# Optimization experiments

Measured on AMD Instinct MI355X. Metric: run time of the kernel, lower is better.

The kernel has to match this reference:

```python
import jax, jax.numpy as jnp
import numpy as np
from jax import lax

EPS = 1e-5
F_IN, F_OUT, R = 128, 256, 16
B, H, W = 16, 128, 128


def _conv(x, w, stride):
    # x: [B,C,H,W], w: [O,I,kh,kw]; ME convs keep coordinates -> SAME padding
    return lax.conv_general_dilated(x, w, (stride, stride), 'SAME',
                                    dimension_numbers=('NCHW', 'OIHW', 'NCHW'))


def _bn(x, g, b, m, v):
    scale = g * lax.rsqrt(v + EPS)
    return x * scale[None, :, None, None] + (b - m * scale)[None, :, None, None]


def setup_inputs() -> dict:
    key = jax.random.key(0)
    ks = jax.random.split(key, 12)
    d = {}
    d['x'] = jax.random.normal(ks[0], (B, F_IN, H, W), jnp.float32)
    # BatchNorm params (eval mode running stats)
    d['bn1_g'] = jax.random.uniform(ks[1], (F_IN,), jnp.float32, 0.5, 1.5)
    d['bn1_b'] = jax.random.normal(ks[2], (F_IN,), jnp.float32) * 0.1
    d['bn1_m'] = jax.random.normal(ks[3], (F_IN,), jnp.float32) * 0.1
    d['bn1_v'] = jax.random.uniform(ks[4], (F_IN,), jnp.float32, 0.5, 1.5)
    d['bn2_g'] = jax.random.uniform(ks[5], (F_OUT,), jnp.float32, 0.5, 1.5)
    d['bn2_b'] = jax.random.normal(ks[6], (F_OUT,), jnp.float32) * 0.1
    d['bn2_m'] = jax.random.normal(ks[7], (F_OUT,), jnp.float32) * 0.1
    d['bn2_v'] = jax.random.uniform(ks[8], (F_OUT,), jnp.float32, 0.5, 1.5)
    # Conv weights (no bias, ME default)
    d['w_conv1'] = jax.random.normal(ks[9], (F_OUT, F_IN, 3, 3), jnp.float32) * (1.0 / np.sqrt(9 * F_IN))
    d['w_conv2'] = jax.random.normal(ks[10], (F_OUT, F_OUT, 3, 3), jnp.float32) * (1.0 / np.sqrt(9 * F_OUT))
    d['w_res'] = jax.random.normal(ks[11], (F_OUT, F_IN, 1, 1), jnp.float32) * (1.0 / np.sqrt(F_IN))
    # SE block linears
    k12, k13, k14, k15 = jax.random.split(jax.random.fold_in(key, 1), 4)
    d['se_w1'] = jax.random.normal(k12, (F_OUT // R, F_OUT), jnp.float32) * (1.0 / np.sqrt(F_OUT))
    d['se_b1'] = jax.random.normal(k13, (F_OUT // R,), jnp.float32) * 0.01
    d['se_w2'] = jax.random.normal(k14, (F_OUT, F_OUT // R), jnp.float32) * (1.0 / np.sqrt(F_OUT // R))
    d['se_b2'] = jax.random.normal(k15, (F_OUT,), jnp.float32) * 0.01
    return d


def reference(x, bn1_g, bn1_b, bn1_m, bn1_v, bn2_g, bn2_b, bn2_m, bn2_v,
              w_conv1, w_conv2, w_res, se_w1, se_b1, se_w2, se_b2):
    # shared BN+ReLU prefix (self.first_batch / self.first_relu reused)
    pre = jax.nn.relu(_bn(x, bn1_g, bn1_b, bn1_m, bn1_v))
    # residual branch: 1x1 stride-2 conv (f_out > f_in)
    residual = _conv(pre, w_res, 2)
    # main branch
    h = _conv(pre, w_conv1, 2)                          # [B,F_OUT,H/2,W/2]
    h = jax.nn.relu(_bn(h, bn2_g, bn2_b, bn2_m, bn2_v))
    h = _conv(h, w_conv2, 1)
    # SE attention: global avg pool -> FC -> ReLU -> FC -> sigmoid -> scale
    s = jnp.mean(h, axis=(2, 3))                        # [B,F_OUT]
    a = jax.nn.sigmoid(jax.nn.relu(s @ se_w1.T + se_b1) @ se_w2.T + se_b2)
    h = h * a[:, :, None, None]
    return h + residual
```

## Files before the change

### kernel.cpp

```cpp
#include <hip/hip_runtime.h>

typedef unsigned short u16;
typedef __attribute__((ext_vector_type(8))) unsigned short u16x8;
typedef __attribute__((ext_vector_type(8))) __bf16 bf16x8;
typedef __attribute__((ext_vector_type(4))) float f32x4;

__device__ __forceinline__ float bf2f(u16 u) {
    return __uint_as_float(((unsigned)u) << 16);
}
__device__ __forceinline__ u16 f2bf(float f) {
    unsigned u = __float_as_uint(f);
    return (u16)((u + 0x7FFFu + ((u >> 16) & 1u)) >> 16);
}

__global__ void setup_kernel(const float* __restrict__ w1, const float* __restrict__ w2,
                             const float* __restrict__ wr,
                             const float* __restrict__ g2, const float* __restrict__ b2,
                             const float* __restrict__ m2, const float* __restrict__ v2,
                             u16* __restrict__ w1t, u16* __restrict__ w2t,
                             u16* __restrict__ wrt, float* __restrict__ bias2f,
                             u16* __restrict__ pre, u16* __restrict__ h1) {
    int b = blockIdx.x;
    if (b < 3585) {
        int i = b * 256 + threadIdx.x;
        if (i < 294912) {
            int ci = i & 127; int t = i >> 7; int o = t & 255; int tap = t >> 8;
            int dy = tap / 3, dx = tap - dy * 3;
            float sc = g2[o] * rsqrtf(v2[o] + 1e-5f);
            w1t[i] = f2bf(w1[((o * 128 + ci) * 3 + dy) * 3 + dx] * sc);
        } else if (i < 294912 + 589824) {
            int j = i - 294912;
            int ci = j & 255; int t = j >> 8; int o = t & 255; int tap = t >> 8;
            int dy = tap / 3, dx = tap - dy * 3;
            w2t[j] = f2bf(w2[((o * 256 + ci) * 3 + dy) * 3 + dx]);
        } else if (i < 294912 + 589824 + 32768) {
            int j = i - (294912 + 589824);
            int ci = j & 127; int o = j >> 7;
            wrt[j] = f2bf(wr[o * 128 + ci]);
        } else {
            int o = i - (294912 + 589824 + 32768);
            if (o < 256) {
                float sc = g2[o] * rsqrtf(v2[o] + 1e-5f);
                bias2f[o] = b2[o] - m2[o] * sc;
            }
        }
    } else if (b < 3585 + 2056) {
        int i = (b - 3585) * 256 + threadIdx.x;
        if (i < 16 * 129 * 128) {
            int c = i & 127; int t = i >> 7; int n = t / 129; int xx = t - n * 129;
            pre[((n * 129 + 128) * 129 + xx) * 128 + c] = 0;
        } else {
            int j = i - 16 * 129 * 128;
            int c = j & 127; int t = j >> 7; int n = t >> 7; int y = t & 127;
            pre[((n * 129 + y) * 129 + 128) * 128 + c] = 0;
        }
    } else {
        int i = (b - (3585 + 2056)) * 256 + threadIdx.x;
        int c = i & 255;
        int t = i >> 8;
        int n = t / 260;
        int cl = t - n * 260;
        int y, x;
        if (cl < 66)       { y = 0;  x = cl; }
        else if (cl < 132) { y = 65; x = cl - 66; }
        else if (cl < 196) { x = 0;  y = cl - 131; }
        else               { x = 65; y = cl - 195; }
        h1[((n * 66 + y) * 66 + x) * 256 + c] = 0;
    }
}

__global__ void pre_kernel(const float* __restrict__ x, const float* __restrict__ g,
                           const float* __restrict__ b, const float* __restrict__ m,
                           const float* __restrict__ v, u16* __restrict__ pre) {
    __shared__ u16 tile[128 * 136];
    int n = blockIdx.x >> 7, y = blockIdx.x & 127;
    int tid = threadIdx.x;
    int c = tid >> 1, xh = (tid & 1) << 6;
    float sc = g[c] * rsqrtf(v[c] + 1e-5f);
    float bi = b[c] - m[c] * sc;
    const float4* src = (const float4*)(x + (((n * 128 + c) * 128 + y) << 7) + xh);
#pragma unroll
    for (int j = 0; j < 16; ++j) {
        float4 val = src[j];
        int xb = xh + j * 4;
        tile[(xb + 0) * 136 + c] = f2bf(fmaxf(val.x * sc + bi, 0.f));
        tile[(xb + 1) * 136 + c] = f2bf(fmaxf(val.y * sc + bi, 0.f));
        tile[(xb + 2) * 136 + c] = f2bf(fmaxf(val.z * sc + bi, 0.f));
        tile[(xb + 3) * 136 + c] = f2bf(fmaxf(val.w * sc + bi, 0.f));
    }
    __syncthreads();
    int c0 = (tid & 15) << 3;
#pragma unroll
    for (int xi = 0; xi < 8; ++xi) {
        int xx = xi * 16 + (tid >> 4);
        u16x8 val = *(const u16x8*)&tile[xx * 136 + c0];
        *(u16x8*)(pre + ((n * 129 + y) * 129 + xx) * 128 + c0) = val;
    }
}

template <int CIN, int NTAPS, int STRIDE, bool BIASRELU, bool POOL>
__global__ __launch_bounds__(512, 2)
void conv_8ph(const u16* __restrict__ in, const u16* __restrict__ wt,
              const float* __restrict__ bias, u16* __restrict__ out,
              float* __restrict__ pool_out,
              int in_row, int in_img, int out_base, int out_row, int out_img) {
    constexpr int CSTEPS = CIN / 64;
    constexpr int KT = CSTEPS * NTAPS;
    __shared__ __attribute__((aligned(16))) u16 lds[81920];

    const int tid = threadIdx.x;
    const int w = tid >> 6, l = tid & 63;
    const int wm = w >> 2, wn = w & 3;
    const int l15 = l & 15;
    const int bid = ((blockIdx.x & 7) << 5) | (blockIdx.x >> 3);
    const int Mbase = bid << 8;

    const int srow = tid >> 3;
    const int swze = (((tid & 7) ^ (srow & 7)) << 3);
    int pix0 = Mbase + srow;
    int nn0 = pix0 >> 12, p0 = (pix0 >> 6) & 63, q0 = pix0 & 63;
    const int abase0 = nn0 * in_img + (STRIDE * p0) * in_row + (STRIDE * q0) * CIN + swze;
    const int astep = STRIDE * in_row;
    const int bbase0 = srow * CIN + swze;
    const int bstep = 64 * CIN;

    int colw[2];
#pragma unroll
    for (int kk = 0; kk < 2; ++kk)
        colw[kk] = (kk * 32 + (l >> 4) * 8) ^ ((l & 7) << 3);

    f32x4 acc[8][4] = {};
    bf16x8 afr[4][2], bXf[2][2], bYf[2][2];

#define AOFF(ks) (((NTAPS == 9) ? ((((ks) / CSTEPS) / 3) * in_row + (((ks) / CSTEPS) % 3) * CIN) : 0) + ((ks) % CSTEPS) * 64)
#define BOFF(ks) (((ks) / CSTEPS) * 256 * CIN + ((ks) % CSTEPS) * 64)
#define GLDS(gsrc, ldst) __builtin_amdgcn_global_load_lds(                          \
        (__attribute__((address_space(1))) void*)(gsrc),                            \
        (__attribute__((address_space(3))) void*)(ldst), 16, 0, 0)
#define STAGE_A(base, h, ks) {                                                      \
    int _ao = AOFF(ks);                                                             \
    GLDS(in + abase0 + (2 * (h) + 0) * astep + _ao,                                 \
         &lds[(base) + (h) * 8192 + 0 * 4096 + w * 512]);                           \
    GLDS(in + abase0 + (2 * (h) + 1) * astep + _ao,                                 \
         &lds[(base) + (h) * 8192 + 1 * 4096 + w * 512]); }
#define STAGE_B(base, h, ks) {                                                      \
    int _bo = BOFF(ks);                                                             \
    GLDS(wt + bbase0 + (2 * (h) + 0) * bstep + _bo,                                 \
         &lds[(base) + (h) * 8192 + 0 * 4096 + w * 512]);                           \
    GLDS(wt + bbase0 + (2 * (h) + 1) * bstep + _bo,                                 \
         &lds[(base) + (h) * 8192 + 1 * 4096 + w * 512]); }
#define BARRIER() { __builtin_amdgcn_s_barrier(); asm volatile("" ::: "memory"); }
#define LDA(base, MH) {                                                             \
    _Pragma("unroll") for (int fm = 0; fm < 4; ++fm)                                \
    _Pragma("unroll") for (int kk = 0; kk < 2; ++kk)                                \
        afr[fm][kk] = *(const bf16x8*)&lds[(base) + ((MH) * 128 + wm * 64 + fm * 16 + l15) * 64 + colw[kk]]; }
#define LDB(base, NH, dst) {                                                        \
    _Pragma("unroll") for (int gn = 0; gn < 2; ++gn)                                \
    _Pragma("unroll") for (int kk = 0; kk < 2; ++kk)                                \
        dst[gn][kk] = *(const bf16x8*)&lds[(base) + ((NH) * 128 + gn * 64 + wn * 16 + l15) * 64 + colw[kk]]; }
#define MFMA_Q(MH, NH, bset) {                                                      \
    _Pragma("unroll") for (int fm = 0; fm < 4; ++fm)                                \
    _Pragma("unroll") for (int gn = 0; gn < 2; ++gn)                                \
    _Pragma("unroll") for (int kk = 0; kk < 2; ++kk)                                \
        acc[(MH) * 4 + fm][(NH) * 2 + gn] = __builtin_amdgcn_mfma_f32_16x16x32_bf16( \
            afr[fm][kk], bset[gn][kk], acc[(MH) * 4 + fm][(NH) * 2 + gn], 0, 0, 0); }

    STAGE_A(0, 0, 0); STAGE_A(0, 1, 0);
    STAGE_B(49152, 0, 0); STAGE_B(49152, 1, 0);
    STAGE_A(16384, 0, 1); STAGE_A(16384, 1, 1);
    asm volatile("s_waitcnt vmcnt(4)" ::: "memory");
    BARRIER();

    int Ar = 0;
    int As = 32768;
    int Brel = 0;

    LDB(49152, 0, bXf);

#define CBODY(T, B0, B1, STAGEA, VM)                                                \
    {                                                                               \
        const int Br = 49152 + Brel, Bs = 49152 + (Brel ^ 16384);                   \
        LDA(Ar, 0);                                                                 \
        LDB(Br, 1, B1);                                                             \
        STAGE_B(Bs, 0, (T) + 1); STAGE_B(Bs, 1, (T) + 1);                           \
        __builtin_amdgcn_s_setprio(1);                                              \
        MFMA_Q(0, 0, B0);                                                           \
        MFMA_Q(0, 1, B1);                                                           \
        __builtin_amdgcn_s_setprio(0);                                              \
        LDA(Ar, 1);                                                                 \
        if (STAGEA) { STAGE_A(As, 0, (T) + 2); STAGE_A(As, 1, (T) + 2); }           \
        __builtin_amdgcn_s_setprio(1);                                              \
        MFMA_Q(1, 1, B1);                                                           \
        __builtin_amdgcn_s_setprio(0);                                              \
        asm volatile("s_waitcnt vmcnt(" #VM ")" ::: "memory");                      \
        BARRIER();                                                                  \
        LDB(49152 + (Brel ^ 16384), 0, B1);         \
        __builtin_amdgcn_s_setprio(1);                                              \
        MFMA_Q(1, 0, B0);                                   \
        __builtin_amdgcn_s_setprio(0);                                              \
        Ar = (Ar == 32768) ? 0 : Ar + 16384;                                        \
        As = (As == 32768) ? 0 : As + 16384;                                        \
        Brel ^= 16384;                                                              \
    }

#pragma unroll 1
    for (int t = 0; t < KT - 2; t += 2) {
        CBODY(t,     bXf, bYf, true, 4);
        CBODY(t + 1, bYf, bXf, true, 4);
    }

    CBODY(KT - 2, bXf, bYf, false, 0);

    {
        const int Br = 49152 + Brel;
        LDA(Ar, 0);
        LDB(Br, 1, bXf);
        MFMA_Q(0, 0, bYf);
        MFMA_Q(0, 1, bXf);
        LDA(Ar, 1);
        MFMA_Q(1, 1, bXf);
        MFMA_Q(1, 0, bYf);
    }
#undef CBODY
#undef AOFF
#undef BOFF
#undef GLDS
#undef STAGE_A
#undef STAGE_B
#undef LDA
#undef LDB

#pragma unroll
    for (int f = 0; f < 8; ++f) {
        const int prow = (f >> 2) * 128 + wm * 64 + (f & 3) * 16 + ((l >> 4) << 2);
#pragma unroll
        for (int g = 0; g < 4; ++g) {
            const int o = (g >> 1) * 128 + (g & 1) * 64 + wn * 16 + l15;
            float bb = 0.f;
            if (BIASRELU) bb = bias[o];
#pragma unroll
            for (int j = 0; j < 4; ++j) {
                int pix = Mbase + prow + j;
                int nn = pix >> 12, p = (pix >> 6) & 63, q = pix & 63;
                float val = acc[f][g][j] + bb;
                if (BIASRELU) val = fmaxf(val, 0.f);
                out[out_base + nn * out_img + p * out_row + q * 256 + o] = f2bf(val);
            }
        }
    }

    if (POOL) {
        float ps[4];
#pragma unroll
        for (int g = 0; g < 4; ++g) {
            float s = 0.f;
#pragma unroll
            for (int f = 0; f < 8; ++f)
#pragma unroll
                for (int j = 0; j < 4; ++j) s += acc[f][g][j];
            s += __shfl_xor(s, 16);
            s += __shfl_xor(s, 32);
            ps[g] = s;
        }
        asm volatile("s_waitcnt lgkmcnt(0)" ::: "memory");
        BARRIER();
        float* fl = (float*)lds;
        if ((l >> 4) == 0) {
#pragma unroll
            for (int g = 0; g < 4; ++g) {
                int o = (g >> 1) * 128 + (g & 1) * 64 + wn * 16 + l15;
                fl[wm * 256 + o] = ps[g];
            }
        }
        BARRIER();
        if (tid < 256)
            pool_out[bid * 256 + tid] = fl[tid] + fl[256 + tid];
    }
#undef MFMA_Q
#undef BARRIER
}

__global__ void se_kernel(const float* __restrict__ partial,
                          const float* __restrict__ w1, const float* __restrict__ b1,
                          const float* __restrict__ w2, const float* __restrict__ b2,
                          float* __restrict__ a) {
    __shared__ float sm[16 * 256];
    __shared__ float hl[16 * 16];
    int t = threadIdx.x;
    for (int n = 0; n < 16; ++n) {
        float s = 0.f;
#pragma unroll
        for (int k = 0; k < 16; ++k) s += partial[(n * 16 + k) * 256 + t];
        sm[n * 256 + t] = s * (1.0f / 4096.0f);
    }
    __syncthreads();
    {
        int bb = t >> 4, j = t & 15;
        float d = b1[j];
        for (int c = 0; c < 256; ++c) d += sm[bb * 256 + c] * w1[j * 256 + c];
        hl[bb * 16 + j] = fmaxf(d, 0.f);
    }
    __syncthreads();
    {
        int o = t;
        for (int bb = 0; bb < 16; ++bb) {
            float z = b2[o];
            for (int j = 0; j < 16; ++j) z += hl[bb * 16 + j] * w2[o * 16 + j];
            a[bb * 256 + o] = 1.0f / (1.0f + expf(-z));
        }
    }
}

__global__ void finalize_kernel(const u16* __restrict__ h2, const u16* __restrict__ res,
                                const float* __restrict__ a, float* __restrict__ out) {
    __shared__ u16 th[256 * 68];
    __shared__ float al[256];
    int n = blockIdx.x >> 6, p = blockIdx.x & 63;
    int t = threadIdx.x;
    al[t] = a[n * 256 + t];
    __syncthreads();
    int o8 = (t & 31) << 3, qr = t >> 5;
    int pixbase = n * 4096 + p * 64;
#pragma unroll
    for (int qi = 0; qi < 8; ++qi) {
        int q = qi * 8 + qr;
        int gi = (pixbase + q) * 256 + o8;
        u16x8 hv = *(const u16x8*)(h2 + gi);
        u16x8 rv = *(const u16x8*)(res + gi);
#pragma unroll
        for (int k = 0; k < 8; ++k) {
            float vv = bf2f(hv[k]) * al[o8 + k] + bf2f(rv[k]);
            th[(o8 + k) * 68 + q] = f2bf(vv);
        }
    }
    __syncthreads();
    int q4 = (t & 15) << 2, ob = t >> 4;
#pragma unroll
    for (int oi = 0; oi < 16; ++oi) {
        int o = oi * 16 + ob;
        float4 vv;
        vv.x = bf2f(th[o * 68 + q4 + 0]);
        vv.y = bf2f(th[o * 68 + q4 + 1]);
        vv.z = bf2f(th[o * 68 + q4 + 2]);
        vv.w = bf2f(th[o * 68 + q4 + 3]);
        *(float4*)(out + ((n * 256 + o) * 64 + p) * 64 + q4) = vv;
    }
}

static const size_t OFF_PRE  = 0;
static const size_t OFF_H1   = 68161536;
static const size_t OFF_RES  = 103845888;
static const size_t OFF_W1T  = 137400320;
static const size_t OFF_W2T  = 137990144;
static const size_t OFF_WRT  = 139169792;
static const size_t OFF_B2F  = 139235328;
static const size_t OFF_PART = 139236352;
static const size_t OFF_A    = 139760640;

extern "C" void kernel_launch(void* const* d_in, const int* in_sizes, int n_in,
                              void* d_out, int out_size, void* d_ws, size_t ws_size,
                              hipStream_t stream) {
    (void)in_sizes; (void)n_in; (void)out_size; (void)ws_size;
    const float* x      = (const float*)d_in[0];
    const float* bn1_g  = (const float*)d_in[1];
    const float* bn1_b  = (const float*)d_in[2];
    const float* bn1_m  = (const float*)d_in[3];
    const float* bn1_v  = (const float*)d_in[4];
    const float* bn2_g  = (const float*)d_in[5];
    const float* bn2_b  = (const float*)d_in[6];
    const float* bn2_m  = (const float*)d_in[7];
    const float* bn2_v  = (const float*)d_in[8];
    const float* wc1    = (const float*)d_in[9];
    const float* wc2    = (const float*)d_in[10];
    const float* wres   = (const float*)d_in[11];
    const float* se_w1  = (const float*)d_in[12];
    const float* se_b1  = (const float*)d_in[13];
    const float* se_w2  = (const float*)d_in[14];
    const float* se_b2  = (const float*)d_in[15];

    char* ws = (char*)d_ws;
    u16*   pre    = (u16*)(ws + OFF_PRE);
    u16*   h2     = (u16*)(ws + OFF_PRE);
    u16*   h1     = (u16*)(ws + OFF_H1);
    u16*   res    = (u16*)(ws + OFF_RES);
    u16*   w1t    = (u16*)(ws + OFF_W1T);
    u16*   w2t    = (u16*)(ws + OFF_W2T);
    u16*   wrt    = (u16*)(ws + OFF_WRT);
    float* bias2f = (float*)(ws + OFF_B2F);
    float* part   = (float*)(ws + OFF_PART);
    float* avec   = (float*)(ws + OFF_A);
    float* out    = (float*)d_out;

    setup_kernel<<<9801, 256, 0, stream>>>(wc1, wc2, wres, bn2_g, bn2_b, bn2_m, bn2_v,
                                           w1t, w2t, wrt, bias2f, pre, h1);
    pre_kernel<<<2048, 256, 0, stream>>>(x, bn1_g, bn1_b, bn1_m, bn1_v, pre);

    conv_8ph<128, 9, 2, true, false><<<256, 512, 0, stream>>>(
        pre, w1t, bias2f, h1, nullptr,
        129 * 128, 129 * 129 * 128,
        67 * 256, 66 * 256, 66 * 66 * 256);

    conv_8ph<128, 1, 2, false, false><<<256, 512, 0, stream>>>(
        pre, wrt, nullptr, res, nullptr,
        129 * 128, 129 * 129 * 128,
        0, 64 * 256, 4096 * 256);

    conv_8ph<256, 9, 1, false, true><<<256, 512, 0, stream>>>(
        h1, w2t, nullptr, h2, part,
        66 * 256, 66 * 66 * 256,
        0, 64 * 256, 4096 * 256);

    se_kernel<<<1, 256, 0, stream>>>(part, se_w1, se_b1, se_w2, se_b2, avec);
    finalize_kernel<<<1024, 256, 0, stream>>>(h2, res, avec, out);
}
```

Baseline: 209.3 us.

## Fuse residual conv and SE into finalize, merge pre-BN into setup

Folds the BN1+ReLU pre-pass into the setup kernel as extra blocks. Computes the 1x1 stride-2 residual conv inside the finalize kernel with MFMA, so the separate residual launch and its bf16 round trip through global memory go away. The single-block SE kernel is also replaced by per-block SE recomputation in finalize. h2 moves to its own buffer because pre must stay live until finalize, and every finalize block now redundantly repeats the SE math and reads pre and weights directly from global memory without LDS staging.

```diff
diff --git a/kernel.cpp b/kernel.cpp
--- a/kernel.cpp
+++ b/kernel.cpp
@@ -13,13 +13,17 @@
     return (u16)((u + 0x7FFFu + ((u >> 16) & 1u)) >> 16);
 }
 
-__global__ void setup_kernel(const float* __restrict__ w1, const float* __restrict__ w2,
+__global__ void setup_kernel(const float* __restrict__ x,
+                             const float* __restrict__ g1, const float* __restrict__ b1,
+                             const float* __restrict__ m1, const float* __restrict__ v1,
+                             const float* __restrict__ w1, const float* __restrict__ w2,
                              const float* __restrict__ wr,
                              const float* __restrict__ g2, const float* __restrict__ b2,
                              const float* __restrict__ m2, const float* __restrict__ v2,
                              u16* __restrict__ w1t, u16* __restrict__ w2t,
                              u16* __restrict__ wrt, float* __restrict__ bias2f,
                              u16* __restrict__ pre, u16* __restrict__ h1) {
+    __shared__ u16 tile[128 * 136];
     int b = blockIdx.x;
     if (b < 3585) {
         int i = b * 256 + threadIdx.x;
@@ -54,47 +58,43 @@
             int c = j & 127; int t = j >> 7; int n = t >> 7; int y = t & 127;
             pre[((n * 129 + y) * 129 + 128) * 128 + c] = 0;
         }
-    } else {
+    } else if (b < 3585 + 2056 + 4160) {
         int i = (b - (3585 + 2056)) * 256 + threadIdx.x;
         int c = i & 255;
         int t = i >> 8;
         int n = t / 260;
         int cl = t - n * 260;
-        int y, x;
-        if (cl < 66)       { y = 0;  x = cl; }
-        else if (cl < 132) { y = 65; x = cl - 66; }
-        else if (cl < 196) { x = 0;  y = cl - 131; }
-        else               { x = 65; y = cl - 195; }
-        h1[((n * 66 + y) * 66 + x) * 256 + c] = 0;
-    }
-}
-
-__global__ void pre_kernel(const float* __restrict__ x, const float* __restrict__ g,
-                           const float* __restrict__ b, const float* __restrict__ m,
-                           const float* __restrict__ v, u16* __restrict__ pre) {
-    __shared__ u16 tile[128 * 136];
-    int n = blockIdx.x >> 7, y = blockIdx.x & 127;
-    int tid = threadIdx.x;
-    int c = tid >> 1, xh = (tid & 1) << 6;
-    float sc = g[c] * rsqrtf(v[c] + 1e-5f);
-    float bi = b[c] - m[c] * sc;
-    const float4* src = (const float4*)(x + (((n * 128 + c) * 128 + y) << 7) + xh);
-#pragma unroll
-    for (int j = 0; j < 16; ++j) {
-        float4 val = src[j];
-        int xb = xh + j * 4;
-        tile[(xb + 0) * 136 + c] = f2bf(fmaxf(val.x * sc + bi, 0.f));
-        tile[(xb + 1) * 136 + c] = f2bf(fmaxf(val.y * sc + bi, 0.f));
-        tile[(xb + 2) * 136 + c] = f2bf(fmaxf(val.z * sc + bi, 0.f));
-        tile[(xb + 3) * 136 + c] = f2bf(fmaxf(val.w * sc + bi, 0.f));
-    }
-    __syncthreads();
-    int c0 = (tid & 15) << 3;
-#pragma unroll
-    for (int xi = 0; xi < 8; ++xi) {
-        int xx = xi * 16 + (tid >> 4);
-        u16x8 val = *(const u16x8*)&tile[xx * 136 + c0];
-        *(u16x8*)(pre + ((n * 129 + y) * 129 + xx) * 128 + c0) = val;
+        int y, x2;
+        if (cl < 66)       { y = 0;  x2 = cl; }
+        else if (cl < 132) { y = 65; x2 = cl - 66; }
+        else if (cl < 196) { x2 = 0; y = cl - 131; }
+        else               { x2 = 65; y = cl - 195; }
+        h1[((n * 66 + y) * 66 + x2) * 256 + c] = 0;
+    } else {
+        int pb = b - (3585 + 2056 + 4160);
+        int n = pb >> 7, y = pb & 127;
+        int tid = threadIdx.x;
+        int c = tid >> 1, xh = (tid & 1) << 6;
+        float sc = g1[c] * rsqrtf(v1[c] + 1e-5f);
+        float bi = b1[c] - m1[c] * sc;
+        const float4* src = (const float4*)(x + (((n * 128 + c) * 128 + y) << 7) + xh);
+#pragma unroll
+        for (int j = 0; j < 16; ++j) {
+            float4 val = src[j];
+            int xb = xh + j * 4;
+            tile[(xb + 0) * 136 + c] = f2bf(fmaxf(val.x * sc + bi, 0.f));
+            tile[(xb + 1) * 136 + c] = f2bf(fmaxf(val.y * sc + bi, 0.f));
+            tile[(xb + 2) * 136 + c] = f2bf(fmaxf(val.z * sc + bi, 0.f));
+            tile[(xb + 3) * 136 + c] = f2bf(fmaxf(val.w * sc + bi, 0.f));
+        }
+        __syncthreads();
+        int c0 = (tid & 15) << 3;
+#pragma unroll
+        for (int xi = 0; xi < 8; ++xi) {
+            int xx = xi * 16 + (tid >> 4);
+            u16x8 val = *(const u16x8*)&tile[xx * 136 + c0];
+            *(u16x8*)(pre + ((n * 129 + y) * 129 + xx) * 128 + c0) = val;
+        }
     }
 }
 
@@ -280,53 +280,84 @@
 #undef BARRIER
 }
 
-__global__ void se_kernel(const float* __restrict__ partial,
-                          const float* __restrict__ w1, const float* __restrict__ b1,
-                          const float* __restrict__ w2, const float* __restrict__ b2,
-                          float* __restrict__ a) {
-    __shared__ float sm[16 * 256];
-    __shared__ float hl[16 * 16];
+__global__ __launch_bounds__(256, 2)
+void finalize_kernel(const u16* __restrict__ h2, const u16* __restrict__ pre,
+                     const u16* __restrict__ wrt, const float* __restrict__ part,
+                     const float* __restrict__ sw1, const float* __restrict__ sb1,
+                     const float* __restrict__ sw2, const float* __restrict__ sb2,
+                     float* __restrict__ out) {
+    __shared__ u16 th[256 * 68];
+    __shared__ u16 resf[64 * 256];
+    __shared__ float al[256];
+    __shared__ float hl[16];
+    int n = blockIdx.x >> 6, p = blockIdx.x & 63;
     int t = threadIdx.x;
-    for (int n = 0; n < 16; ++n) {
+    const int w = t >> 6, l = t & 63;
+    const int l15 = l & 15, lk = (l >> 4) << 3;
+
+    f32x4 racc[4][4] = {};
+    {
+        const u16* pbase = pre + ((n * 129 + 2 * p) * 129) * 128;
+#pragma unroll
+        for (int ks = 0; ks < 4; ++ks) {
+            bf16x8 af[4], bf[4];
+#pragma unroll
+            for (int fm = 0; fm < 4; ++fm) {
+                int q = fm * 16 + l15;
+                af[fm] = *(const bf16x8*)(pbase + (2 * q) * 128 + ks * 32 + lk);
+            }
+#pragma unroll
+            for (int fn = 0; fn < 4; ++fn) {
+                int o = w * 64 + fn * 16 + l15;
+                bf[fn] = *(const bf16x8*)(wrt + o * 128 + ks * 32 + lk);
+            }
+#pragma unroll
+            for (int fm = 0; fm < 4; ++fm)
+#pragma unroll
+                for (int fn = 0; fn < 4; ++fn)
+                    racc[fm][fn] = __builtin_amdgcn_mfma_f32_16x16x32_bf16(
+                        af[fm], bf[fn], racc[fm][fn], 0, 0, 0);
+        }
+#pragma unroll
+        for (int fm = 0; fm < 4; ++fm)
+#pragma unroll
+            for (int fn = 0; fn < 4; ++fn)
+#pragma unroll
+                for (int j = 0; j < 4; ++j)
+                    resf[(fm * 16 + ((l >> 4) << 2) + j) * 256 + w * 64 + fn * 16 + l15] =
+                        f2bf(racc[fm][fn][j]);
+    }
+
+    {
         float s = 0.f;
 #pragma unroll
-        for (int k = 0; k < 16; ++k) s += partial[(n * 16 + k) * 256 + t];
-        sm[n * 256 + t] = s * (1.0f / 4096.0f);
+        for (int k = 0; k < 16; ++k) s += part[(n * 16 + k) * 256 + t];
+        al[t] = s * (1.0f / 4096.0f);
+    }
+    __syncthreads();
+    if (t < 16) {
+        float d = sb1[t];
+        for (int c = 0; c < 256; ++c) d += al[c] * sw1[t * 256 + c];
+        hl[t] = fmaxf(d, 0.f);
     }
     __syncthreads();
     {
-        int bb = t >> 4, j = t & 15;
-        float d = b1[j];
-        for (int c = 0; c < 256; ++c) d += sm[bb * 256 + c] * w1[j * 256 + c];
-        hl[bb * 16 + j] = fmaxf(d, 0.f);
+        float z = sb2[t];
+#pragma unroll
+        for (int j = 0; j < 16; ++j) z += hl[j] * sw2[t * 16 + j];
+        float a_t = 1.0f / (1.0f + expf(-z));
+        __syncthreads();
+        al[t] = a_t;
     }
     __syncthreads();
-    {
-        int o = t;
-        for (int bb = 0; bb < 16; ++bb) {
-            float z = b2[o];
-            for (int j = 0; j < 16; ++j) z += hl[bb * 16 + j] * w2[o * 16 + j];
-            a[bb * 256 + o] = 1.0f / (1.0f + expf(-z));
-        }
-    }
-}
-
-__global__ void finalize_kernel(const u16* __restrict__ h2, const u16* __restrict__ res,
-                                const float* __restrict__ a, float* __restrict__ out) {
-    __shared__ u16 th[256 * 68];
-    __shared__ float al[256];
-    int n = blockIdx.x >> 6, p = blockIdx.x & 63;
-    int t = threadIdx.x;
-    al[t] = a[n * 256 + t];
-    __syncthreads();
+
     int o8 = (t & 31) << 3, qr = t >> 5;
     int pixbase = n * 4096 + p * 64;
 #pragma unroll
     for (int qi = 0; qi < 8; ++qi) {
         int q = qi * 8 + qr;
-        int gi = (pixbase + q) * 256 + o8;
-        u16x8 hv = *(const u16x8*)(h2 + gi);
-        u16x8 rv = *(const u16x8*)(res + gi);
+        u16x8 hv = *(const u16x8*)(h2 + (pixbase + q) * 256 + o8);
+        u16x8 rv = *(const u16x8*)(resf + q * 256 + o8);
 #pragma unroll
         for (int k = 0; k < 8; ++k) {
             float vv = bf2f(hv[k]) * al[o8 + k] + bf2f(rv[k]);
@@ -349,13 +380,12 @@
 
 static const size_t OFF_PRE  = 0;
 static const size_t OFF_H1   = 68161536;
-static const size_t OFF_RES  = 103845888;
+static const size_t OFF_H2   = 103845888;
 static const size_t OFF_W1T  = 137400320;
 static const size_t OFF_W2T  = 137990144;
 static const size_t OFF_WRT  = 139169792;
 static const size_t OFF_B2F  = 139235328;
 static const size_t OFF_PART = 139236352;
-static const size_t OFF_A    = 139760640;
 
 extern "C" void kernel_launch(void* const* d_in, const int* in_sizes, int n_in,
                               void* d_out, int out_size, void* d_ws, size_t ws_size,
@@ -380,36 +410,29 @@
 
     char* ws = (char*)d_ws;
     u16*   pre    = (u16*)(ws + OFF_PRE);
-    u16*   h2     = (u16*)(ws + OFF_PRE);
     u16*   h1     = (u16*)(ws + OFF_H1);
-    u16*   res    = (u16*)(ws + OFF_RES);
+    u16*   h2     = (u16*)(ws + OFF_H2);
     u16*   w1t    = (u16*)(ws + OFF_W1T);
     u16*   w2t    = (u16*)(ws + OFF_W2T);
     u16*   wrt    = (u16*)(ws + OFF_WRT);
     float* bias2f = (float*)(ws + OFF_B2F);
     float* part   = (float*)(ws + OFF_PART);
-    float* avec   = (float*)(ws + OFF_A);
     float* out    = (float*)d_out;
 
-    setup_kernel<<<9801, 256, 0, stream>>>(wc1, wc2, wres, bn2_g, bn2_b, bn2_m, bn2_v,
-                                           w1t, w2t, wrt, bias2f, pre, h1);
-    pre_kernel<<<2048, 256, 0, stream>>>(x, bn1_g, bn1_b, bn1_m, bn1_v, pre);
+    setup_kernel<<<11849, 256, 0, stream>>>(x, bn1_g, bn1_b, bn1_m, bn1_v,
+                                            wc1, wc2, wres, bn2_g, bn2_b, bn2_m, bn2_v,
+                                            w1t, w2t, wrt, bias2f, pre, h1);
 
     conv_8ph<128, 9, 2, true, false><<<256, 512, 0, stream>>>(
         pre, w1t, bias2f, h1, nullptr,
         129 * 128, 129 * 129 * 128,
         67 * 256, 66 * 256, 66 * 66 * 256);
 
-    conv_8ph<128, 1, 2, false, false><<<256, 512, 0, stream>>>(
-        pre, wrt, nullptr, res, nullptr,
-        129 * 128, 129 * 129 * 128,
-        0, 64 * 256, 4096 * 256);
-
     conv_8ph<256, 9, 1, false, true><<<256, 512, 0, stream>>>(
         h1, w2t, nullptr, h2, part,
         66 * 256, 66 * 66 * 256,
         0, 64 * 256, 4096 * 256);
 
-    se_kernel<<<1, 256, 0, stream>>>(part, se_w1, se_b1, se_w2, se_b2, avec);
-    finalize_kernel<<<1024, 256, 0, stream>>>(h2, res, avec, out);
-}
+    finalize_kernel<<<1024, 256, 0, stream>>>(h2, pre, wrt, part,
+                                              se_w1, se_b1, se_w2, se_b2, out);
+}
```

Result: faster. 201.6 us (-3.7%).
